# Optimization experiments

Measured on AMD Instinct MI355X. Metric: run time of the kernel, lower is better.

The kernel has to match this reference:

```python
import jax, jax.numpy as jnp
import numpy as np

N_PART = 256
N_DIM = 3
HIDDEN = 512


def _xavier(k, shape):
    # matches nn.initializers.xavier_uniform() on the (in, out) trailing dims
    fan_in, fan_out = shape[-2], shape[-1]
    lim = float(np.sqrt(6.0 / (fan_in + fan_out)))
    return jax.random.uniform(k, shape, jnp.float32, -lim, lim)


def setup_inputs() -> dict:
    key = jax.random.key(0)
    ks = jax.random.split(key, 4)
    x = jax.random.normal(ks[0], (N_PART, N_DIM), jnp.float32)
    # ConvLocal(1x1) on input (n_part, 1, n_part, C): one unique (C_in, C_out)
    # weight matrix per spatial location w in [0, n_part).
    W0 = _xavier(ks[1], (N_PART, N_DIM, HIDDEN))
    b0 = jnp.zeros((N_PART, HIDDEN), jnp.float32)
    W1 = _xavier(ks[2], (N_PART, HIDDEN, HIDDEN))
    b1 = jnp.zeros((N_PART, HIDDEN), jnp.float32)
    W2 = _xavier(ks[3], (N_PART, HIDDEN, 1))
    b2 = jnp.zeros((N_PART, 1), jnp.float32)
    return {"x": x, "W0": W0, "b0": b0, "W1": W1, "b1": b1, "W2": W2, "b2": b2}


def reference(x, W0, b0, W1, b1, W2, b2):
    n_part = x.shape[0]
    # repeat+reshape in the original makes h[b, w, :] = x[b, :] for every w;
    # fold that broadcast directly into the first per-location matmul.
    h = jnp.tanh(jnp.einsum('bc,wcf->bwf', x, W0) + b0)           # (B, W, H)
    h = jnp.tanh(jnp.einsum('bwc,wcf->bwf', h, W1) + b1)          # (B, W, H)
    h = jnp.einsum('bwc,wcf->bwf', h, W2) + b2                    # last_activation=False
    slater = h.reshape(n_part, n_part).T                          # (n_part, n_part)
    sign, logdet = jnp.linalg.slogdet(slater)
    return (sign.reshape(()), logdet.reshape(()))
```

## Files before the change

kernel.cpp:

```cpp
#include <hip/hip_runtime.h>
#include <math.h>

#define NP 256
#define HID 512
#define KB 8

typedef short bf16x8 __attribute__((ext_vector_type(8)));
typedef float f32x4v __attribute__((ext_vector_type(4)));

__device__ __forceinline__ short bf16_rne(float v, float& rem) {
    unsigned u = __float_as_uint(v);
    unsigned r = (u + 0x7FFFu + ((u >> 16) & 1u)) & 0xFFFF0000u;
    rem = v - __uint_as_float(r);
    return (short)(r >> 16);
}
__device__ __forceinline__ void split3(float v, short& h, short& m, short& lo) {
    float r1, r2;
    h = bf16_rne(v, r1);
    m = bf16_rne(r1, r2);
    unsigned u2 = __float_as_uint(r2);
    lo = (short)((u2 + 0x7FFFu + ((u2 >> 16) & 1u)) >> 16);
}

__global__ __launch_bounds__(512, 1) void k_mlp_v4(
    const float* __restrict__ x,  const float* __restrict__ W0,
    const float* __restrict__ b0, const float* __restrict__ W1,
    const float* __restrict__ b1, const float* __restrict__ W2,
    const float* __restrict__ b2, float* __restrict__ slater)
{
    __shared__ __align__(16) short pA[3][2][4][128][8];
    __shared__ float s_red[8][128];
    const int bid  = blockIdx.x;
    const int xcd  = bid & 7;
    const int jj   = bid >> 3;
    const int half = jj & 1;
    const int w    = (xcd << 5) + (jj >> 1);
    const int tid  = threadIdx.x;
    const int wid  = tid >> 6;
    const int l    = tid & 63;
    const int col  = l & 15;
    const int g    = l >> 4;
    const int fb   = wid * 64;

    f32x4v acc[8][4];
    #pragma unroll
    for (int bt = 0; bt < 8; ++bt)
        #pragma unroll
        for (int ft = 0; ft < 4; ++ft)
            acc[bt][ft] = (f32x4v){0.f, 0.f, 0.f, 0.f};

    const int bb = tid & 127;
    const int co = tid >> 7;
    const int bg = half*128 + bb;
    const float x0 = x[bg*3+0], x1 = x[bg*3+1], x2 = x[bg*3+2];
    const float* W0w = W0 + (size_t)w*3*HID;
    const float* b0w = b0 + (size_t)w*HID;
    const float* w1c = W1 + (size_t)w*HID*HID + fb + 4*col;

    for (int ph = 0; ph < 8; ++ph) {
        if (ph) __syncthreads();
        #pragma unroll 4
        for (int pass = 0; pass < 16; ++pass) {
            int cl = co + 4*pass;
            int c  = ph*64 + cl;
            float v = x0*W0w[c] + x1*W0w[HID+c] + x2*W0w[2*HID+c] + b0w[c];
            float t = tanhf(v);
            short h, m, lo; split3(t, h, m, lo);
            int ks = cl >> 5, r32 = cl & 31;
            int gg = (r32 >> 2) & 3;
            int jv = (r32 & 3) + 4*(r32 >> 4);
            pA[0][ks][gg][bb][jv] = h;
            pA[1][ks][gg][bb][jv] = m;
            pA[2][ks][gg][bb][jv] = lo;
        }
        __syncthreads();

        #pragma unroll
        for (int ks = 0; ks < 2; ++ks) {
            bf16x8 Bh[4], Bm[4], Bl[4];
            const float* bkp = w1c + (size_t)(ph*64 + ks*32 + 4*g)*HID;
            #pragma unroll
            for (int j = 0; j < 8; ++j) {
                int koff = (j&3) + 16*(j>>2);
                float4 bv = *reinterpret_cast<const float4*>(bkp + (size_t)koff*HID);
                short h, m, lo;
                split3(bv.x, h, m, lo); Bh[0][j]=h; Bm[0][j]=m; Bl[0][j]=lo;
                split3(bv.y, h, m, lo); Bh[1][j]=h; Bm[1][j]=m; Bl[1][j]=lo;
                split3(bv.z, h, m, lo); Bh[2][j]=h; Bm[2][j]=m; Bl[2][j]=lo;
                split3(bv.w, h, m, lo); Bh[3][j]=h; Bm[3][j]=m; Bl[3][j]=lo;
            }
            #pragma unroll
            for (int btc = 0; btc < 2; ++btc) {
                bf16x8 Ah[4], Am[4], Al[4];
                #pragma unroll
                for (int b4 = 0; b4 < 4; ++b4) {
                    int row = (btc*4 + b4)*16 + col;
                    Ah[b4] = *reinterpret_cast<const bf16x8*>(&pA[0][ks][g][row][0]);
                    Am[b4] = *reinterpret_cast<const bf16x8*>(&pA[1][ks][g][row][0]);
                    Al[b4] = *reinterpret_cast<const bf16x8*>(&pA[2][ks][g][row][0]);
                }
                #pragma unroll
                for (int b4 = 0; b4 < 4; ++b4) {
                    const int bt = btc*4 + b4;
                    #pragma unroll
                    for (int ft = 0; ft < 4; ++ft) {
                        acc[bt][ft] = __builtin_amdgcn_mfma_f32_16x16x32_bf16(Ah[b4], Bh[ft], acc[bt][ft], 0,0,0);
                        acc[bt][ft] = __builtin_amdgcn_mfma_f32_16x16x32_bf16(Ah[b4], Bm[ft], acc[bt][ft], 0,0,0);
                        acc[bt][ft] = __builtin_amdgcn_mfma_f32_16x16x32_bf16(Am[b4], Bh[ft], acc[bt][ft], 0,0,0);
                        acc[bt][ft] = __builtin_amdgcn_mfma_f32_16x16x32_bf16(Ah[b4], Bl[ft], acc[bt][ft], 0,0,0);
                        acc[bt][ft] = __builtin_amdgcn_mfma_f32_16x16x32_bf16(Am[b4], Bm[ft], acc[bt][ft], 0,0,0);
                        acc[bt][ft] = __builtin_amdgcn_mfma_f32_16x16x32_bf16(Al[b4], Bh[ft], acc[bt][ft], 0,0,0);
                    }
                }
            }
        }
    }

    const float* b1w = b1 + (size_t)w*HID + fb + 4*col;
    const float* W2w = W2 + (size_t)w*HID + fb + 4*col;
    float4 bb4 = *reinterpret_cast<const float4*>(b1w);
    float4 wt4 = *reinterpret_cast<const float4*>(W2w);
    float bbv[4] = {bb4.x, bb4.y, bb4.z, bb4.w};
    float wtv[4] = {wt4.x, wt4.y, wt4.z, wt4.w};
    #pragma unroll
    for (int bt = 0; bt < 8; ++bt)
        #pragma unroll
        for (int r = 0; r < 4; ++r) {
            float part = 0.f;
            #pragma unroll
            for (int ft = 0; ft < 4; ++ft)
                part += tanhf(acc[bt][ft][r] + bbv[ft]) * wtv[ft];
            part += __shfl_xor(part, 1); part += __shfl_xor(part, 2);
            part += __shfl_xor(part, 4); part += __shfl_xor(part, 8);
            if (col == 0) s_red[wid][bt*16 + g*4 + r] = part;
        }
    __syncthreads();
    if (tid < 128) {
        float s = 0.f;
        #pragma unroll
        for (int wd = 0; wd < 8; ++wd) s += s_red[wd][tid];
        slater[w*NP + half*128 + tid] = s + b2[w];
    }
}

__device__ __forceinline__ float rf_f32(float x) {
    return __uint_as_float(__builtin_amdgcn_readfirstlane(__float_as_uint(x)));
}
__device__ __forceinline__ float rl_f32(float x, int lane) {
    return __uint_as_float(__builtin_amdgcn_readlane(__float_as_uint(x), lane));
}
template<int CTRL>
__device__ __forceinline__ unsigned dpp_u32(unsigned v) {
    return (unsigned)__builtin_amdgcn_update_dpp(0, (int)v, CTRL, 0xF, 0xF, true);
}

__global__ __launch_bounds__(512, 1) void k_lu_blk(const float* __restrict__ A,
                                                   float* __restrict__ out)
{
    const int tid  = threadIdx.x;
    const int ln   = tid & 63;
    const int wv   = tid >> 6;
    const int cb   = wv * 32;

    __shared__ float s_panel[2][NP][KB+1];
    __shared__ float s_stage[2*KB][260];
    __shared__ float s_U[KB][260];
    __shared__ int   s_src[NP];
    __shared__ int   s_p[KB];
    __shared__ int   s_uslot[KB];
    __shared__ float s_piv[NP];

    float a[4][32];
    {
        const float4* Ap = reinterpret_cast<const float4*>(A);
        #pragma unroll
        for (int q = 0; q < 4; ++q)
            #pragma unroll
            for (int u = 0; u < 8; ++u) {
                float4 v = Ap[(q*64+ln)*64 + wv*8 + u];
                a[q][u*4+0]=v.x; a[q][u*4+1]=v.y; a[q][u*4+2]=v.z; a[q][u*4+3]=v.w;
            }
    }

    auto STAGE = [&](int k0s, float (*spnl)[KB+1]) {
        switch ((k0s & 31) >> 3) {
            case 0:
                #pragma unroll
                for (int q = 0; q < 4; ++q)
                    #pragma unroll
                    for (int c = 0; c < KB; ++c) spnl[q*64+ln][c] = a[q][c];
                break;
            case 1:
                #pragma unroll
                for (int q = 0; q < 4; ++q)
                    #pragma unroll
                    for (int c = 0; c < KB; ++c) spnl[q*64+ln][c] = a[q][8+c];
                break;
            case 2:
                #pragma unroll
                for (int q = 0; q < 4; ++q)
                    #pragma unroll
                    for (int c = 0; c < KB; ++c) spnl[q*64+ln][c] = a[q][16+c];
                break;
            default:
                #pragma unroll
                for (int q = 0; q < 4; ++q)
                    #pragma unroll
                    for (int c = 0; c < KB; ++c) spnl[q*64+ln][c] = a[q][24+c];
                break;
        }
    };

    auto STEP2 = [&](int k0, float (*spnl)[KB+1]) {
        const int lane = tid;
        float pa[4][KB];
        int   lid[4];
        #pragma unroll
        for (int q = 0; q < 4; ++q) {
            lid[q] = q*64 + lane;
            #pragma unroll
            for (int c = 0; c < KB; ++c) pa[q][c] = spnl[q*64+lane][c];
        }
        int pvt[KB];
        #pragma unroll
        for (int kk = 0; kk < KB; ++kk) {
            const int k = k0 + kk;
            unsigned key = 0u;
            #pragma unroll
            for (int q = 0; q < 4; ++q) {
                unsigned ab = __float_as_uint(pa[q][kk]) & 0x7FFFFFFFu;
                unsigned kq = (ab & 0xFFFFFF00u) | (unsigned)(255 - lid[q]);
                if (lid[q] >= k && kq > key) key = kq;
            }
            { unsigned t;
              t = dpp_u32<0x111>(key); if (t > key) key = t;
              t = dpp_u32<0x112>(key); if (t > key) key = t;
              t = dpp_u32<0x114>(key); if (t > key) key = t;
              t = dpp_u32<0x118>(key); if (t > key) key = t;
              t = dpp_u32<0x142>(key); if (t > key) key = t;
              t = dpp_u32<0x143>(key); if (t > key) key = t;
            }
            const unsigned gk = (unsigned)__builtin_amdgcn_readlane((int)key, 63);
            const int p = 255 - (int)(gk & 0xFFu);
            pvt[kk] = p;
            int myslot = -1;
            #pragma unroll
            for (int q = 0; q < 4; ++q) if (lid[q] == p) myslot = q;
            unsigned long long bal = __ballot(myslot >= 0);
            const int plane = (int)__ffsll((long long)bal) - 1;
            const int pslot = __builtin_amdgcn_readlane(myslot, plane);
            float urow[KB];
            #pragma unroll
            for (int c = 0; c < KB; ++c) {
                float t = (pslot==0) ? pa[0][c] : (pslot==1) ? pa[1][c]
                        : (pslot==2) ? pa[2][c] : pa[3][c];
                urow[c] = rl_f32(t, plane);
            }
            #pragma unroll
            for (int q = 0; q < 4; ++q) {
                int lq = lid[q];
                lid[q] = (lq == k) ? p : (lq == p) ? k : lq;
            }
            const float pv = urow[kk];
            if (lane == 0) s_piv[k] = (p != k) ? -pv : pv;
            const float rp = rf_f32(1.0f / pv);
            #pragma unroll
            for (int q = 0; q < 4; ++q)
                if (lid[q] > k) pa[q][kk] *= rp;
            #pragma unroll
            for (int c = kk+1; c < KB; ++c) {
                #pragma unroll
                for (int q = 0; q < 4; ++q)
                    if (lid[q] > k) pa[q][c] = fmaf(-pa[q][kk], urow[c], pa[q][c]);
            }
        }
        #pragma unroll
        for (int q = 0; q < 4; ++q)
            #pragma unroll
            for (int c = 0; c < KB; ++c) spnl[lid[q]][c] = pa[q][c];
        if (lane == 0) {
            s_p[0]=pvt[0]; s_p[1]=pvt[1]; s_p[2]=pvt[2]; s_p[3]=pvt[3];
            s_p[4]=pvt[4]; s_p[5]=pvt[5]; s_p[6]=pvt[6]; s_p[7]=pvt[7];
        }
        int l8 = lane - 8;
        int psel = pvt[0];
        psel = (l8==1)?pvt[1]:psel; psel = (l8==2)?pvt[2]:psel;
        psel = (l8==3)?pvt[3]:psel; psel = (l8==4)?pvt[4]:psel;
        psel = (l8==5)?pvt[5]:psel; psel = (l8==6)?pvt[6]:psel;
        psel = (l8==7)?pvt[7]:psel;
        const int mypos = (lane < 8) ? (k0 + lane) : psel;
        int cur = mypos;
        #pragma unroll
        for (int s = 0; s < KB; ++s) {
            int cA = __builtin_amdgcn_readlane(cur, s);
            int cB = __builtin_amdgcn_readlane(cur, 8+s);
            int ks = k0 + s, ps = pvt[s];
            if (mypos == ks) cur = cB;
            else if (mypos == ps) cur = cA;
        }
        if (lane < 16) s_src[mypos] = cur;
        if (lane < 8) {
            int c = cur, slot = 8;
            slot = (pvt[0]==c)? 8:slot; slot = (pvt[1]==c)? 9:slot;
            slot = (pvt[2]==c)?10:slot; slot = (pvt[3]==c)?11:slot;
            slot = (pvt[4]==c)?12:slot; slot = (pvt[5]==c)?13:slot;
            slot = (pvt[6]==c)?14:slot; slot = (pvt[7]==c)?15:slot;
            if (c >= k0 && c < k0+KB) slot = c - k0;
            s_uslot[lane] = slot;
        }
    };

    if (tid < 256) s_src[tid] = tid;
    if (wv == 0) STAGE(0, s_panel[0]);
    __syncthreads();
    if (tid < 64) STEP2(0, s_panel[0]);
    __syncthreads();

    for (int pi = 0; pi < 31; ++pi) {
        const int k0  = pi * KB;
        const int buf = pi & 1;
        const int nk  = k0 + KB;

        int pp[KB];
        #pragma unroll
        for (int s = 0; s < KB; ++s) pp[s] = s_p[s];

        #pragma unroll
        for (int q = 0; q < 4; ++q) {
            const int iq = q*64 + ln;
            if (iq >= k0 && iq < nk) {
                const int sl = iq - k0;
                #pragma unroll
                for (int u = 0; u < 8; ++u) {
                    float4 v; v.x=a[q][u*4+0]; v.y=a[q][u*4+1];
                    v.z=a[q][u*4+2]; v.w=a[q][u*4+3];
                    *reinterpret_cast<float4*>(&s_stage[sl][cb + u*4]) = v;
                }
            }
            #pragma unroll
            for (int s = 0; s < KB; ++s) {
                if (iq == pp[s]) {
                    #pragma unroll
                    for (int u = 0; u < 8; ++u) {
                        float4 v; v.x=a[q][u*4+0]; v.y=a[q][u*4+1];
                        v.z=a[q][u*4+2]; v.w=a[q][u*4+3];
                        *reinterpret_cast<float4*>(&s_stage[KB+s][cb + u*4]) = v;
                    }
                }
            }
        }
        __syncthreads();

        #pragma unroll
        for (int q = 0; q < 4; ++q) {
            const int iq = q*64 + ln;
            const int sr = s_src[iq];
            if (sr != iq) {
                int slot = KB;
                #pragma unroll
                for (int s = 0; s < KB; ++s) slot = (pp[s]==sr) ? KB+s : slot;
                if (sr >= k0 && sr < nk) slot = sr - k0;
                #pragma unroll
                for (int u = 0; u < 8; ++u) {
                    float4 v = *reinterpret_cast<const float4*>(&s_stage[slot][cb + u*4]);
                    a[q][u*4+0]=v.x; a[q][u*4+1]=v.y; a[q][u*4+2]=v.z; a[q][u*4+3]=v.w;
                }
            }
        }
        if (tid < 256) {
            const int j = tid;
            int us[KB];
            #pragma unroll
            for (int m = 0; m < KB; ++m) us[m] = s_uslot[m];
            float uv[KB];
            #pragma unroll
            for (int m = 0; m < KB; ++m) {
                float v = s_stage[us[m]][j];
                #pragma unroll
                for (int s = 0; s < KB; ++s)
                    if (s < m) v = fmaf(-s_panel[buf][k0+m][s], uv[s], v);
                uv[m] = v;
                s_U[m][j] = v;
            }
        }
        __syncthreads();

        if (tid < 256) s_src[tid] = tid;
        if (wv == (nk >> 5)) {
            float L0[4][KB];
            #pragma unroll
            for (int q = 0; q < 4; ++q)
                #pragma unroll
                for (int m = 0; m < KB; ++m) L0[q][m] = s_panel[buf][q*64+ln][m];
            #pragma unroll
            for (int u4 = 0; u4 < 8; ++u4) {
                if (cb + u4*4 >= nk && cb + u4*4 < nk + KB) {
                    #pragma unroll
                    for (int m = 0; m < KB; ++m) {
                        const float4 uvv = *reinterpret_cast<const float4*>(&s_U[m][cb + u4*4]);
                        #pragma unroll
                        for (int q = 0; q < 4; ++q) {
                            if (q*64 + 63 >= nk) {
                                a[q][u4*4+0] = fmaf(-L0[q][m], uvv.x, a[q][u4*4+0]);
                                a[q][u4*4+1] = fmaf(-L0[q][m], uvv.y, a[q][u4*4+1]);
                                a[q][u4*4+2] = fmaf(-L0[q][m], uvv.z, a[q][u4*4+2]);
                                a[q][u4*4+3] = fmaf(-L0[q][m], uvv.w, a[q][u4*4+3]);
                            }
                        }
                    }
                }
            }
            STAGE(nk, s_panel[buf ^ 1]);
        }
        __syncthreads();

        if (tid < 64) STEP2(nk, s_panel[buf ^ 1]);
        if (cb + 31 >= nk + KB) {
            float L0[4][KB];
            #pragma unroll
            for (int q = 0; q < 4; ++q)
                #pragma unroll
                for (int m = 0; m < KB; ++m) L0[q][m] = s_panel[buf][q*64+ln][m];
            #pragma unroll
            for (int u4 = 0; u4 < 8; ++u4) {
                if (cb + u4*4 >= nk + KB) {
                    #pragma unroll
                    for (int m = 0; m < KB; ++m) {
                        const float4 uvv = *reinterpret_cast<const float4*>(&s_U[m][cb + u4*4]);
                        #pragma unroll
                        for (int q = 0; q < 4; ++q) {
                            if (q*64 + 63 >= nk) {
                                a[q][u4*4+0] = fmaf(-L0[q][m], uvv.x, a[q][u4*4+0]);
                                a[q][u4*4+1] = fmaf(-L0[q][m], uvv.y, a[q][u4*4+1]);
                                a[q][u4*4+2] = fmaf(-L0[q][m], uvv.z, a[q][u4*4+2]);
                                a[q][u4*4+3] = fmaf(-L0[q][m], uvv.w, a[q][u4*4+3]);
                            }
                        }
                    }
                }
            }
        }
        __syncthreads();
    }

    if (tid < 64) {
        double ld = 0.0; int neg = 0;
        #pragma unroll
        for (int q = 0; q < 4; ++q) {
            float pv = s_piv[q*64 + tid];
            ld  += (double)logf(fabsf(pv));
            neg ^= (pv < 0.0f) ? 1 : 0;
        }
        #pragma unroll
        for (int off = 32; off; off >>= 1) {
            ld  += __shfl_xor(ld, off);
            neg ^= __shfl_xor(neg, off);
        }
        if (tid == 0) { out[0] = neg ? -1.0f : 1.0f; out[1] = (float)ld; }
    }
}

extern "C" void kernel_launch(void* const* d_in, const int* in_sizes, int n_in,
                              void* d_out, int out_size, void* d_ws, size_t ws_size,
                              hipStream_t stream)
{
    const float* x  = (const float*)d_in[0];
    const float* W0 = (const float*)d_in[1];
    const float* b0 = (const float*)d_in[2];
    const float* W1 = (const float*)d_in[3];
    const float* b1 = (const float*)d_in[4];
    const float* W2 = (const float*)d_in[5];
    const float* b2 = (const float*)d_in[6];
    float* out    = (float*)d_out;
    float* slater = (float*)d_ws;

    k_mlp_v4<<<512, 512, 0, stream>>>(x, W0, b0, W1, b1, W2, b2, slater);
    k_lu_blk<<<1, 512, 0, stream>>>(slater, out);
}
```

Measured before the change: 655.0 us.

## Widen LU panel to 16 and move panel factorization to a dedicated wave

```diff
diff --git a/kernel.cpp b/kernel.cpp
--- a/kernel.cpp
+++ b/kernel.cpp
@@ -3,7 +3,7 @@
 
 #define NP 256
 #define HID 512
-#define KB 8
+#define KB 16
 
 typedef short bf16x8 __attribute__((ext_vector_type(8)));
 typedef float f32x4v __attribute__((ext_vector_type(4)));
@@ -154,13 +154,14 @@
     return (unsigned)__builtin_amdgcn_update_dpp(0, (int)v, CTRL, 0xF, 0xF, true);
 }
 
-__global__ __launch_bounds__(512, 1) void k_lu_blk(const float* __restrict__ A,
+__global__ __launch_bounds__(576, 1) void k_lu_blk(const float* __restrict__ A,
                                                    float* __restrict__ out)
 {
     const int tid  = threadIdx.x;
     const int ln   = tid & 63;
     const int wv   = tid >> 6;
-    const int cb   = wv * 32;
+    const int cb   = (wv & 7) * 32;
+    const bool data = (tid < 512);
 
     __shared__ float s_panel[2][NP][KB+1];
     __shared__ float s_stage[2*KB][260];
@@ -171,7 +172,7 @@
     __shared__ float s_piv[NP];
 
     float a[4][32];
-    {
+    if (data) {
         const float4* Ap = reinterpret_cast<const float4*>(A);
         #pragma unroll
         for (int q = 0; q < 4; ++q)
@@ -183,36 +184,21 @@
     }
 
     auto STAGE = [&](int k0s, float (*spnl)[KB+1]) {
-        switch ((k0s & 31) >> 3) {
-            case 0:
-                #pragma unroll
-                for (int q = 0; q < 4; ++q)
-                    #pragma unroll
-                    for (int c = 0; c < KB; ++c) spnl[q*64+ln][c] = a[q][c];
-                break;
-            case 1:
-                #pragma unroll
-                for (int q = 0; q < 4; ++q)
-                    #pragma unroll
-                    for (int c = 0; c < KB; ++c) spnl[q*64+ln][c] = a[q][8+c];
-                break;
-            case 2:
-                #pragma unroll
-                for (int q = 0; q < 4; ++q)
-                    #pragma unroll
-                    for (int c = 0; c < KB; ++c) spnl[q*64+ln][c] = a[q][16+c];
-                break;
-            default:
-                #pragma unroll
-                for (int q = 0; q < 4; ++q)
-                    #pragma unroll
-                    for (int c = 0; c < KB; ++c) spnl[q*64+ln][c] = a[q][24+c];
-                break;
+        if (((k0s >> 4) & 1) == 0) {
+            #pragma unroll
+            for (int q = 0; q < 4; ++q)
+                #pragma unroll
+                for (int c = 0; c < KB; ++c) spnl[q*64+ln][c] = a[q][c];
+        } else {
+            #pragma unroll
+            for (int q = 0; q < 4; ++q)
+                #pragma unroll
+                for (int c = 0; c < KB; ++c) spnl[q*64+ln][c] = a[q][16+c];
         }
     };
 
     auto STEP2 = [&](int k0, float (*spnl)[KB+1]) {
-        const int lane = tid;
+        const int lane = ln;
         float pa[4][KB];
         int   lid[4];
         #pragma unroll
@@ -279,44 +265,40 @@
             #pragma unroll
             for (int c = 0; c < KB; ++c) spnl[lid[q]][c] = pa[q][c];
         if (lane == 0) {
-            s_p[0]=pvt[0]; s_p[1]=pvt[1]; s_p[2]=pvt[2]; s_p[3]=pvt[3];
-            s_p[4]=pvt[4]; s_p[5]=pvt[5]; s_p[6]=pvt[6]; s_p[7]=pvt[7];
-        }
-        int l8 = lane - 8;
+            #pragma unroll
+            for (int s = 0; s < KB; ++s) s_p[s] = pvt[s];
+        }
+        const int l16 = lane - KB;
         int psel = pvt[0];
-        psel = (l8==1)?pvt[1]:psel; psel = (l8==2)?pvt[2]:psel;
-        psel = (l8==3)?pvt[3]:psel; psel = (l8==4)?pvt[4]:psel;
-        psel = (l8==5)?pvt[5]:psel; psel = (l8==6)?pvt[6]:psel;
-        psel = (l8==7)?pvt[7]:psel;
-        const int mypos = (lane < 8) ? (k0 + lane) : psel;
+        #pragma unroll
+        for (int s = 1; s < KB; ++s) psel = (l16 == s) ? pvt[s] : psel;
+        const int mypos = (lane < KB) ? (k0 + lane) : psel;
         int cur = mypos;
         #pragma unroll
         for (int s = 0; s < KB; ++s) {
             int cA = __builtin_amdgcn_readlane(cur, s);
-            int cB = __builtin_amdgcn_readlane(cur, 8+s);
+            int cB = __builtin_amdgcn_readlane(cur, KB+s);
             int ks = k0 + s, ps = pvt[s];
             if (mypos == ks) cur = cB;
             else if (mypos == ps) cur = cA;
         }
-        if (lane < 16) s_src[mypos] = cur;
-        if (lane < 8) {
-            int c = cur, slot = 8;
-            slot = (pvt[0]==c)? 8:slot; slot = (pvt[1]==c)? 9:slot;
-            slot = (pvt[2]==c)?10:slot; slot = (pvt[3]==c)?11:slot;
-            slot = (pvt[4]==c)?12:slot; slot = (pvt[5]==c)?13:slot;
-            slot = (pvt[6]==c)?14:slot; slot = (pvt[7]==c)?15:slot;
+        if (lane < 2*KB) s_src[mypos] = cur;
+        if (lane < KB) {
+            int c = cur, slot = KB;
+            #pragma unroll
+            for (int s = 0; s < KB; ++s) slot = (pvt[s]==c) ? KB+s : slot;
             if (c >= k0 && c < k0+KB) slot = c - k0;
             s_uslot[lane] = slot;
         }
     };
 
     if (tid < 256) s_src[tid] = tid;
-    if (wv == 0) STAGE(0, s_panel[0]);
+    if (data && wv == 0) STAGE(0, s_panel[0]);
     __syncthreads();
-    if (tid < 64) STEP2(0, s_panel[0]);
+    if (!data) STEP2(0, s_panel[0]);
     __syncthreads();
 
-    for (int pi = 0; pi < 31; ++pi) {
+    for (int pi = 0; pi < 15; ++pi) {
         const int k0  = pi * KB;
         const int buf = pi & 1;
         const int nk  = k0 + KB;
@@ -325,57 +307,58 @@
         #pragma unroll
         for (int s = 0; s < KB; ++s) pp[s] = s_p[s];
 
-        #pragma unroll
-        for (int q = 0; q < 4; ++q) {
-            const int iq = q*64 + ln;
-            if (iq >= k0 && iq < nk) {
-                const int sl = iq - k0;
-                #pragma unroll
-                for (int u = 0; u < 8; ++u) {
-                    float4 v; v.x=a[q][u*4+0]; v.y=a[q][u*4+1];
-                    v.z=a[q][u*4+2]; v.w=a[q][u*4+3];
-                    *reinterpret_cast<float4*>(&s_stage[sl][cb + u*4]) = v;
-                }
-            }
-            #pragma unroll
-            for (int s = 0; s < KB; ++s) {
-                if (iq == pp[s]) {
+        if (data) {
+            #pragma unroll
+            for (int q = 0; q < 4; ++q) {
+                const int iq = q*64 + ln;
+                if (iq >= k0 && iq < nk) {
+                    const int sl = iq - k0;
                     #pragma unroll
                     for (int u = 0; u < 8; ++u) {
                         float4 v; v.x=a[q][u*4+0]; v.y=a[q][u*4+1];
                         v.z=a[q][u*4+2]; v.w=a[q][u*4+3];
-                        *reinterpret_cast<float4*>(&s_stage[KB+s][cb + u*4]) = v;
+                        *reinterpret_cast<float4*>(&s_stage[sl][cb + u*4]) = v;
+                    }
+                }
+                #pragma unroll
+                for (int s = 0; s < KB; ++s) {
+                    if (iq == pp[s]) {
+                        #pragma unroll
+                        for (int u = 0; u < 8; ++u) {
+                            float4 v; v.x=a[q][u*4+0]; v.y=a[q][u*4+1];
+                            v.z=a[q][u*4+2]; v.w=a[q][u*4+3];
+                            *reinterpret_cast<float4*>(&s_stage[KB+s][cb + u*4]) = v;
+                        }
                     }
                 }
             }
         }
         __syncthreads();
 
-        #pragma unroll
-        for (int q = 0; q < 4; ++q) {
-            const int iq = q*64 + ln;
-            const int sr = s_src[iq];
-            if (sr != iq) {
-                int slot = KB;
-                #pragma unroll
-                for (int s = 0; s < KB; ++s) slot = (pp[s]==sr) ? KB+s : slot;
-                if (sr >= k0 && sr < nk) slot = sr - k0;
-                #pragma unroll
-                for (int u = 0; u < 8; ++u) {
-                    float4 v = *reinterpret_cast<const float4*>(&s_stage[slot][cb + u*4]);
-                    a[q][u*4+0]=v.x; a[q][u*4+1]=v.y; a[q][u*4+2]=v.z; a[q][u*4+3]=v.w;
+        if (data) {
+            #pragma unroll
+            for (int q = 0; q < 4; ++q) {
+                const int iq = q*64 + ln;
+                const int sr = s_src[iq];
+                if (sr != iq) {
+                    int slot = KB;
+                    #pragma unroll
+                    for (int s = 0; s < KB; ++s) slot = (pp[s]==sr) ? KB+s : slot;
+                    if (sr >= k0 && sr < nk) slot = sr - k0;
+                    #pragma unroll
+                    for (int u = 0; u < 8; ++u) {
+                        float4 v = *reinterpret_cast<const float4*>(&s_stage[slot][cb + u*4]);
+                        a[q][u*4+0]=v.x; a[q][u*4+1]=v.y; a[q][u*4+2]=v.z; a[q][u*4+3]=v.w;
+                    }
                 }
             }
         }
         if (tid < 256) {
             const int j = tid;
-            int us[KB];
-            #pragma unroll
-            for (int m = 0; m < KB; ++m) us[m] = s_uslot[m];
             float uv[KB];
             #pragma unroll
             for (int m = 0; m < KB; ++m) {
-                float v = s_stage[us[m]][j];
+                float v = s_stage[s_uslot[m]][j];
                 #pragma unroll
                 for (int s = 0; s < KB; ++s)
                     if (s < m) v = fmaf(-s_panel[buf][k0+m][s], uv[s], v);
@@ -386,25 +369,23 @@
         __syncthreads();
 
         if (tid < 256) s_src[tid] = tid;
-        if (wv == (nk >> 5)) {
-            float L0[4][KB];
-            #pragma unroll
-            for (int q = 0; q < 4; ++q)
-                #pragma unroll
-                for (int m = 0; m < KB; ++m) L0[q][m] = s_panel[buf][q*64+ln][m];
-            #pragma unroll
-            for (int u4 = 0; u4 < 8; ++u4) {
-                if (cb + u4*4 >= nk && cb + u4*4 < nk + KB) {
-                    #pragma unroll
-                    for (int m = 0; m < KB; ++m) {
+        if (data && wv == (nk >> 5)) {
+            #pragma unroll
+            for (int m = 0; m < KB; ++m) {
+                float Lm[4];
+                #pragma unroll
+                for (int q = 0; q < 4; ++q) Lm[q] = s_panel[buf][q*64+ln][m];
+                #pragma unroll
+                for (int u4 = 0; u4 < 8; ++u4) {
+                    if (cb + u4*4 >= nk && cb + u4*4 < nk + KB) {
                         const float4 uvv = *reinterpret_cast<const float4*>(&s_U[m][cb + u4*4]);
                         #pragma unroll
                         for (int q = 0; q < 4; ++q) {
                             if (q*64 + 63 >= nk) {
-                                a[q][u4*4+0] = fmaf(-L0[q][m], uvv.x, a[q][u4*4+0]);
-                                a[q][u4*4+1] = fmaf(-L0[q][m], uvv.y, a[q][u4*4+1]);
-                                a[q][u4*4+2] = fmaf(-L0[q][m], uvv.z, a[q][u4*4+2]);
-                                a[q][u4*4+3] = fmaf(-L0[q][m], uvv.w, a[q][u4*4+3]);
+                                a[q][u4*4+0] = fmaf(-Lm[q], uvv.x, a[q][u4*4+0]);
+                                a[q][u4*4+1] = fmaf(-Lm[q], uvv.y, a[q][u4*4+1]);
+                                a[q][u4*4+2] = fmaf(-Lm[q], uvv.z, a[q][u4*4+2]);
+                                a[q][u4*4+3] = fmaf(-Lm[q], uvv.w, a[q][u4*4+3]);
                             }
                         }
                     }
@@ -414,26 +395,24 @@
         }
         __syncthreads();
 
-        if (tid < 64) STEP2(nk, s_panel[buf ^ 1]);
-        if (cb + 31 >= nk + KB) {
-            float L0[4][KB];
-            #pragma unroll
-            for (int q = 0; q < 4; ++q)
-                #pragma unroll
-                for (int m = 0; m < KB; ++m) L0[q][m] = s_panel[buf][q*64+ln][m];
-            #pragma unroll
-            for (int u4 = 0; u4 < 8; ++u4) {
-                if (cb + u4*4 >= nk + KB) {
-                    #pragma unroll
-                    for (int m = 0; m < KB; ++m) {
+        if (!data) STEP2(nk, s_panel[buf ^ 1]);
+        if (data && cb + 31 >= nk + KB) {
+            #pragma unroll
+            for (int m = 0; m < KB; ++m) {
+                float Lm[4];
+                #pragma unroll
+                for (int q = 0; q < 4; ++q) Lm[q] = s_panel[buf][q*64+ln][m];
+                #pragma unroll
+                for (int u4 = 0; u4 < 8; ++u4) {
+                    if (cb + u4*4 >= nk + KB) {
                         const float4 uvv = *reinterpret_cast<const float4*>(&s_U[m][cb + u4*4]);
                         #pragma unroll
                         for (int q = 0; q < 4; ++q) {
                             if (q*64 + 63 >= nk) {
-                                a[q][u4*4+0] = fmaf(-L0[q][m], uvv.x, a[q][u4*4+0]);
-                                a[q][u4*4+1] = fmaf(-L0[q][m], uvv.y, a[q][u4*4+1]);
-                                a[q][u4*4+2] = fmaf(-L0[q][m], uvv.z, a[q][u4*4+2]);
-                                a[q][u4*4+3] = fmaf(-L0[q][m], uvv.w, a[q][u4*4+3]);
+                                a[q][u4*4+0] = fmaf(-Lm[q], uvv.x, a[q][u4*4+0]);
+                                a[q][u4*4+1] = fmaf(-Lm[q], uvv.y, a[q][u4*4+1]);
+                                a[q][u4*4+2] = fmaf(-Lm[q], uvv.z, a[q][u4*4+2]);
+                                a[q][u4*4+3] = fmaf(-Lm[q], uvv.w, a[q][u4*4+3]);
                             }
                         }
                     }
@@ -475,5 +454,5 @@
     float* slater = (float*)d_ws;
 
     k_mlp_v4<<<512, 512, 0, stream>>>(x, W0, b0, W1, b1, W2, b2, slater);
-    k_lu_blk<<<1, 512, 0, stream>>>(slater, out);
-}
+    k_lu_blk<<<1, 576, 0, stream>>>(slater, out);
+}
```

Result: slower. 834.9 us (+27.5%).
